# Performance work log

Measured on AMD Instinct MI355X. Metric: run time of the kernel, lower is better.

Reference implementation:

```python
import jax, jax.numpy as jnp
import numpy as np

BASE_CHUNK = 64
MAX_SEQ_LEN = 256
HIDDEN = 128
DIST_CORE = 6.0
DIST_SHELL = 10.0


def _linear_params(key, fan_in, fan_out):
    lim = 1.0 / np.sqrt(fan_in)
    kw, kb = jax.random.split(key)
    W = jax.random.uniform(kw, (fan_in, fan_out), jnp.float32, -lim, lim)
    b = jax.random.uniform(kb, (fan_out,), jnp.float32, -lim, lim)
    return W, b


def setup_inputs() -> dict:
    key = jax.random.key(0)
    ks = jax.random.split(key, 8)
    B, S, De = 16, 768, 16
    node_features = jax.random.normal(ks[0], (B, S, HIDDEN), jnp.float32)
    # channel 0 acts as a pairwise distance; uniform in [0, 20) spans core/shell thresholds
    edge_features = jax.random.uniform(ks[1], (B, S, S, De), jnp.float32) * 20.0
    sequence_mask = jnp.ones((B, S), jnp.float32)
    pocket_mask = jax.random.bernoulli(ks[2], 0.02, (B, S))
    W_node, b_node = _linear_params(ks[3], HIDDEN, 32)
    W_e1, b_e1 = _linear_params(ks[4], 1, 64)
    W_e2, b_e2 = _linear_params(ks[5], 64, 32)
    W_imp, b_imp = _linear_params(ks[6], 64, 1)
    return dict(node_features=node_features, edge_features=edge_features,
                sequence_mask=sequence_mask, pocket_mask=pocket_mask,
                W_node=W_node, b_node=b_node, W_e1=W_e1, b_e1=b_e1,
                W_e2=W_e2, b_e2=b_e2, W_imp=W_imp, b_imp=b_imp)


def reference(node_features, edge_features, sequence_mask, pocket_mask,
              W_node, b_node, W_e1, b_e1, W_e2, b_e2, W_imp, b_imp):
    B, S, _ = node_features.shape
    adj = min(BASE_CHUNK, MAX_SEQ_LEN // 4) if S > MAX_SEQ_LEN else BASE_CHUNK  # static

    node_enc = node_features @ W_node + b_node                      # [B,S,32]
    edge_summary = edge_features.mean(axis=-1).mean(axis=-1)[..., None]  # [B,S,1]
    h = jax.nn.relu(edge_summary @ W_e1 + b_e1)                     # [B,S,64]
    edge_enc = h @ W_e2 + b_e2                                      # [B,S,32]
    combined = jnp.concatenate([node_enc, edge_enc], axis=-1)       # [B,S,64]
    importance = jax.nn.sigmoid(combined @ W_imp + b_imp) * sequence_mask[..., None]  # [B,S,1]
    imp = importance[..., 0]                                        # [B,S]

    # ---- pocket branch (vectorized over batch) ----
    # min distance from each node to any pocket node (inf where no pocket)
    dist = jnp.where(pocket_mask[:, None, :], edge_features[..., 0], jnp.inf).min(axis=2)  # [B,S]
    core = dist < DIST_CORE
    imp_mean = imp.mean(axis=1, keepdims=True)
    shell = (dist >= DIST_CORE) & (dist < DIST_SHELL) & (imp > imp_mean)
    merged = pocket_mask | core | shell
    merged_len = jnp.minimum(merged.sum(axis=1), MAX_SEQ_LEN)       # clamp (argsort path keeps max_seq_len)
    chunk_pocket = jnp.minimum(jnp.maximum(merged_len, adj), MAX_SEQ_LEN).astype(jnp.float32)

    # ---- no-pocket branch ----
    imp_full = importance.mean(axis=(1, 2))                          # [B]
    chunk_np = jnp.clip(BASE_CHUNK * imp_full,
                        float(adj // 2), float(min(adj * 2, MAX_SEQ_LEN)))

    has_pocket = pocket_mask.any(axis=1)
    chunk_sizes = jnp.where(has_pocket, chunk_pocket, chunk_np)      # [B]
    return chunk_sizes, MAX_SEQ_LEN
```

## Files before the change

### kernel.cpp

```cpp
#include <hip/hip_runtime.h>
#include <hip/hip_bf16.h>
#include <math.h>

#define BB 16
#define SS 768
#define DE 16
#define HID 128


__global__ __launch_bounds__(256) void sniff_kernel(const unsigned int* __restrict__ pm,
                                                    int* __restrict__ flag) {
    __shared__ int bad;
    int tid = threadIdx.x;
    if (tid == 0) bad = 0;
    __syncthreads();
    for (int t = tid; t < (BB * SS) / 4; t += 256) {
        unsigned int w = pm[t];
        if (w > 1u && w != 0x3F800000u) bad = 1;
    }
    __syncthreads();
    if (tid == 0) *flag = bad;
}

__global__ __launch_bounds__(128) void precompute_kernel(
    const float* __restrict__ Wn, const float* __restrict__ bn,
    const float* __restrict__ We2, const float* __restrict__ be2,
    const float* __restrict__ Wimp, const float* __restrict__ bimp,
    float* __restrict__ ws) {
    int tid = threadIdx.x;
    if (tid < 128) {
        float s = 0.f;
        for (int c = 0; c < 32; ++c) s += Wn[tid * 32 + c] * Wimp[c];
        ws[16 + tid] = s;
    }
    if (tid < 64) {
        float s = 0.f;
        for (int c = 0; c < 32; ++c) s += We2[tid * 32 + c] * Wimp[32 + c];
        ws[144 + tid] = s;
    }
    if (tid == 0) {
        float s = bimp[0];
        for (int c = 0; c < 32; ++c) s += bn[c] * Wimp[c];
        for (int c = 0; c < 32; ++c) s += be2[c] * Wimp[32 + c];
        ws[208] = s;
    }
}

__global__ __launch_bounds__(256) void edge_kernel(
    const float4* __restrict__ edge, const float* __restrict__ nf,
    const void* __restrict__ pmask, const float* __restrict__ seqmask,
    const float* __restrict__ We1, const float* __restrict__ be1,
    float* __restrict__ ws) {
    const int tid = threadIdx.x;
    const int bi = blockIdx.x;
    const int b = bi / SS;

    __shared__ float s_a[256];
    __shared__ float s_b[256];
    __shared__ unsigned char s_m[SS];

    const int flag = ((const int*)ws)[0];
    if (flag) {
        const unsigned char* pm = (const unsigned char*)pmask + (size_t)b * SS;
        for (int j = tid; j < SS; j += 256) s_m[j] = pm[j] ? 1 : 0;
    } else {
        const unsigned int* pm = (const unsigned int*)pmask + (size_t)b * SS;
        for (int j = tid; j < SS; j += 256) s_m[j] = pm[j] ? 1 : 0;
    }
    __syncthreads();

    const float4* row = edge + (size_t)bi * (SS * DE / 4);
    float sum = 0.f;
    float dmin = INFINITY;
#pragma unroll
    for (int it = 0; it < 12; ++it) {
        int t = tid + it * 256;
        float4 v = row[t];
        sum += (v.x + v.y) + (v.z + v.w);
        if ((t & 3) == 0) {
            if (s_m[t >> 2]) dmin = fminf(dmin, v.x);
        }
    }
    s_a[tid] = sum;
    s_b[tid] = dmin;
    __syncthreads();
    for (int off = 128; off > 0; off >>= 1) {
        if (tid < off) {
            s_a[tid] += s_a[tid + off];
            s_b[tid] = fminf(s_b[tid], s_b[tid + off]);
        }
        __syncthreads();
    }
    const float total = s_a[0];
    const float dall = s_b[0];
    __syncthreads();

    const float es = total * (1.0f / (float)(SS * DE));
    float p = 0.f;
    if (tid < 128) p += nf[(size_t)bi * HID + tid] * ws[16 + tid];
    if (tid < 64) {
        float h = es * We1[tid] + be1[tid];
        h = fmaxf(h, 0.f);
        p += h * ws[144 + tid];
    }
    s_a[tid] = p;
    __syncthreads();
    for (int off = 128; off > 0; off >>= 1) {
        if (tid < off) s_a[tid] += s_a[tid + off];
        __syncthreads();
    }
    if (tid == 0) {
        float logit = s_a[0] + ws[208];
        float impv = seqmask[bi] / (1.f + expf(-logit));
        ws[256 + bi] = impv;
        ws[256 + BB * SS + bi] = dall;
    }
}

__global__ __launch_bounds__(256) void final_kernel(
    const void* __restrict__ pmask, const float* __restrict__ ws,
    float* __restrict__ out) {
    const int tid = threadIdx.x;
    const int b = blockIdx.x;
    __shared__ float s_f[256];
    __shared__ int s_i[256];

    const float* imp = ws + 256;
    const float* dist = ws + 256 + BB * SS;
    const int flag = ((const int*)ws)[0];

    float psum = 0.f;
    int por = 0;
    for (int i = tid; i < SS; i += 256) {
        psum += imp[b * SS + i];
        int m = flag ? (((const unsigned char*)pmask)[b * SS + i] != 0)
                     : (((const unsigned int*)pmask)[b * SS + i] != 0u);
        por |= m;
    }
    s_f[tid] = psum;
    s_i[tid] = por;
    __syncthreads();
    for (int off = 128; off > 0; off >>= 1) {
        if (tid < off) {
            s_f[tid] += s_f[tid + off];
            s_i[tid] |= s_i[tid + off];
        }
        __syncthreads();
    }
    const float imp_mean = s_f[0] / (float)SS;
    const int haspocket = s_i[0];
    __syncthreads();

    int cnt = 0;
    for (int i = tid; i < SS; i += 256) {
        int m = flag ? (((const unsigned char*)pmask)[b * SS + i] != 0)
                     : (((const unsigned int*)pmask)[b * SS + i] != 0u);
        float d = dist[b * SS + i];
        bool core = d < 6.0f;
        bool shell = (d >= 6.0f) && (d < 10.0f) && (imp[b * SS + i] > imp_mean);
        cnt += (m || core || shell) ? 1 : 0;
    }
    s_i[tid] = cnt;
    __syncthreads();
    for (int off = 128; off > 0; off >>= 1) {
        if (tid < off) s_i[tid] += s_i[tid + off];
        __syncthreads();
    }
    if (tid == 0) {
        float chunk;
        if (haspocket) {
            float ml = fminf((float)s_i[0], 256.f);
            chunk = fminf(fmaxf(ml, 64.f), 256.f);
        } else {
            chunk = fminf(fmaxf(64.f * imp_mean, 32.f), 128.f);
        }
        out[b] = chunk;
        if (b == 0) out[BB] = 256.f;
    }
}

extern "C" void kernel_launch(void* const* d_in, const int* in_sizes, int n_in,
                              void* d_out, int out_size, void* d_ws, size_t ws_size,
                              hipStream_t stream) {
    const float* nf = (const float*)d_in[0];
    const float4* edge = (const float4*)d_in[1];
    const float* seqmask = (const float*)d_in[2];
    const void* pmask = d_in[3];
    const float* Wn = (const float*)d_in[4];
    const float* bn = (const float*)d_in[5];
    const float* We1 = (const float*)d_in[6];
    const float* be1 = (const float*)d_in[7];
    const float* We2 = (const float*)d_in[8];
    const float* be2 = (const float*)d_in[9];
    const float* Wimp = (const float*)d_in[10];
    const float* bimp = (const float*)d_in[11];
    float* ws = (float*)d_ws;
    float* out = (float*)d_out;

    sniff_kernel<<<1, 256, 0, stream>>>((const unsigned int*)pmask, (int*)ws);
    precompute_kernel<<<1, 128, 0, stream>>>(Wn, bn, We2, be2, Wimp, bimp, ws);
    edge_kernel<<<BB * SS, 256, 0, stream>>>(edge, nf, pmask, seqmask, We1, be1, ws);
    final_kernel<<<BB, 256, 0, stream>>>(pmask, ws, out);
}
```

Baseline: 789.9 us.

## Assign one wavefront per edge row and merge setup kernels

The edge kernel now processes four rows per block, one 64-lane wavefront per row. Block-wide shared-memory tree reductions with repeated __syncthreads are replaced by wavefront shuffle reductions. The sniff and precompute kernels are folded into one setup kernel, saving a launch. Each block also loads the pocket mask once for four rows instead of once per row. The workload is bandwidth-bound (about 755 MB of edge data), so the gain may be limited to reduced sync and launch overhead.

```diff
diff --git a/kernel.cpp b/kernel.cpp
--- a/kernel.cpp
+++ b/kernel.cpp
@@ -8,26 +8,20 @@
 #define HID 128
 
 
-__global__ __launch_bounds__(256) void sniff_kernel(const unsigned int* __restrict__ pm,
-                                                    int* __restrict__ flag) {
+__global__ __launch_bounds__(256) void setup_kernel(
+    const unsigned int* __restrict__ pm,
+    const float* __restrict__ Wn, const float* __restrict__ bn,
+    const float* __restrict__ We2, const float* __restrict__ be2,
+    const float* __restrict__ Wimp, const float* __restrict__ bimp,
+    float* __restrict__ ws) {
+    int tid = threadIdx.x;
     __shared__ int bad;
-    int tid = threadIdx.x;
     if (tid == 0) bad = 0;
     __syncthreads();
     for (int t = tid; t < (BB * SS) / 4; t += 256) {
         unsigned int w = pm[t];
         if (w > 1u && w != 0x3F800000u) bad = 1;
     }
-    __syncthreads();
-    if (tid == 0) *flag = bad;
-}
-
-__global__ __launch_bounds__(128) void precompute_kernel(
-    const float* __restrict__ Wn, const float* __restrict__ bn,
-    const float* __restrict__ We2, const float* __restrict__ be2,
-    const float* __restrict__ Wimp, const float* __restrict__ bimp,
-    float* __restrict__ ws) {
-    int tid = threadIdx.x;
     if (tid < 128) {
         float s = 0.f;
         for (int c = 0; c < 32; ++c) s += Wn[tid * 32 + c] * Wimp[c];
@@ -44,6 +38,8 @@
         for (int c = 0; c < 32; ++c) s += be2[c] * Wimp[32 + c];
         ws[208] = s;
     }
+    __syncthreads();
+    if (tid == 0) ((int*)ws)[0] = bad;
 }
 
 __global__ __launch_bounds__(256) void edge_kernel(
@@ -52,13 +48,13 @@
     const float* __restrict__ We1, const float* __restrict__ be1,
     float* __restrict__ ws) {
     const int tid = threadIdx.x;
-    const int bi = blockIdx.x;
-    const int b = bi / SS;
+    const int wave = tid >> 6;
+    const int lane = tid & 63;
+    const int bi0 = blockIdx.x * 4;
+    const int b = bi0 / SS;
+    const int bi = bi0 + wave;
 
-    __shared__ float s_a[256];
-    __shared__ float s_b[256];
     __shared__ unsigned char s_m[SS];
-
     const int flag = ((const int*)ws)[0];
     if (flag) {
         const unsigned char* pm = (const unsigned char*)pmask + (size_t)b * SS;
@@ -72,48 +68,32 @@
     const float4* row = edge + (size_t)bi * (SS * DE / 4);
     float sum = 0.f;
     float dmin = INFINITY;
-#pragma unroll
-    for (int it = 0; it < 12; ++it) {
-        int t = tid + it * 256;
-        float4 v = row[t];
+#pragma unroll 8
+    for (int k = 0; k < 48; ++k) {
+        const int t = lane + (k << 6);
+        const float4 v = row[t];
         sum += (v.x + v.y) + (v.z + v.w);
-        if ((t & 3) == 0) {
+        if ((lane & 3) == 0) {
             if (s_m[t >> 2]) dmin = fminf(dmin, v.x);
         }
     }
-    s_a[tid] = sum;
-    s_b[tid] = dmin;
-    __syncthreads();
-    for (int off = 128; off > 0; off >>= 1) {
-        if (tid < off) {
-            s_a[tid] += s_a[tid + off];
-            s_b[tid] = fminf(s_b[tid], s_b[tid + off]);
-        }
-        __syncthreads();
+    for (int off = 32; off > 0; off >>= 1) {
+        sum += __shfl_down(sum, off, 64);
+        dmin = fminf(dmin, __shfl_down(dmin, off, 64));
     }
-    const float total = s_a[0];
-    const float dall = s_b[0];
-    __syncthreads();
+    sum = __shfl(sum, 0, 64);
 
-    const float es = total * (1.0f / (float)(SS * DE));
-    float p = 0.f;
-    if (tid < 128) p += nf[(size_t)bi * HID + tid] * ws[16 + tid];
-    if (tid < 64) {
-        float h = es * We1[tid] + be1[tid];
-        h = fmaxf(h, 0.f);
-        p += h * ws[144 + tid];
-    }
-    s_a[tid] = p;
-    __syncthreads();
-    for (int off = 128; off > 0; off >>= 1) {
-        if (tid < off) s_a[tid] += s_a[tid + off];
-        __syncthreads();
-    }
-    if (tid == 0) {
-        float logit = s_a[0] + ws[208];
-        float impv = seqmask[bi] / (1.f + expf(-logit));
-        ws[256 + bi] = impv;
-        ws[256 + BB * SS + bi] = dall;
+    const float es = sum * (1.0f / (float)(SS * DE));
+    float p = nf[(size_t)bi * HID + lane] * ws[16 + lane]
+            + nf[(size_t)bi * HID + 64 + lane] * ws[16 + 64 + lane];
+    float h = fmaxf(es * We1[lane] + be1[lane], 0.f);
+    p += h * ws[144 + lane];
+    for (int off = 32; off > 0; off >>= 1) p += __shfl_down(p, off, 64);
+
+    if (lane == 0) {
+        const float logit = p + ws[208];
+        ws[256 + bi] = seqmask[bi] / (1.f + expf(-logit));
+        ws[256 + BB * SS + bi] = __shfl(dmin, 0, 64);
     }
 }
 
@@ -197,8 +177,9 @@
     float* ws = (float*)d_ws;
     float* out = (float*)d_out;
 
-    sniff_kernel<<<1, 256, 0, stream>>>((const unsigned int*)pmask, (int*)ws);
-    precompute_kernel<<<1, 128, 0, stream>>>(Wn, bn, We2, be2, Wimp, bimp, ws);
-    edge_kernel<<<BB * SS, 256, 0, stream>>>(edge, nf, pmask, seqmask, We1, be1, ws);
+    setup_kernel<<<1, 256, 0, stream>>>((const unsigned int*)pmask, Wn, bn,
+                                        We2, be2, Wimp, bimp, ws);
+    edge_kernel<<<BB * SS / 4, 256, 0, stream>>>(edge, nf, pmask, seqmask,
+                                                 We1, be1, ws);
     final_kernel<<<BB, 256, 0, stream>>>(pmask, ws, out);
 }
```

Measured after the change: 795.4 us. About the same (+0.7%).
